# Performance work log

Measured on AMD Instinct MI355X. Metric: run time of the kernel, lower is better.

The kernel has to match this reference:

```python
import jax, jax.numpy as jnp
import numpy as np

ALPHA = 0.2          # LeakyReLU negative slope
NEG_INF = -9e15      # mask fill value, matches torch source
ADJ_EPS = 1e-6       # clamp min for log(adj)


def setup_inputs() -> dict:
    key = jax.random.key(0)
    k1, k2, k3, k4, k5 = jax.random.split(key, 5)
    N, F_IN, H, D = 4096, 256, 4, 64  # out_features = H*D = 256
    h = jax.random.normal(k1, (N, F_IN), dtype=jnp.float32)
    # xavier_uniform-ish scale for W (gain 1.414)
    limW = 1.414 * np.sqrt(6.0 / (F_IN + D))
    W = jax.random.uniform(k2, (H, F_IN, D), dtype=jnp.float32, minval=-limW, maxval=limW)
    lima = 1.414 * np.sqrt(6.0 / (D + 1))
    a_src = jax.random.uniform(k3, (H, D, 1), dtype=jnp.float32, minval=-lima, maxval=lima)
    a_dst = jax.random.uniform(k4, (H, D, 1), dtype=jnp.float32, minval=-lima, maxval=lima)
    # random 0/1 dense adjacency (float, as the torch module takes log(adj))
    adj = jax.random.randint(k5, (N, N), 0, 2).astype(jnp.float32)
    return {"h": h, "adj": adj, "W": W, "a_src": a_src, "a_dst": a_dst}


def reference(h, adj, W, a_src, a_dst):
    N = h.shape[0]
    # Wh: (H, N, D)
    Wh = jnp.einsum('ni,hid->hnd', h, W)
    # per-node source/dest scores: (H, N, 1)
    attn_src = jnp.einsum('hnd,hdo->hno', Wh, a_src)
    attn_dst = jnp.einsum('hnd,hdo->hno', Wh, a_dst)
    # broadcast to dense (H, N, N) logits
    e = jax.nn.leaky_relu(attn_src + jnp.swapaxes(attn_dst, -1, -2), negative_slope=ALPHA)
    adj_b = adj[None]  # (1, N, N)
    attention = jnp.where(adj_b > 0, e + jnp.log(jnp.maximum(adj_b, ADJ_EPS)), NEG_INF)
    attention = jax.nn.softmax(attention, axis=-1)
    # dropout p=0.0 (eval) -> identity
    h_prime = jnp.einsum('hnm,hmd->hnd', attention, Wh)        # (H, N, D)
    h_prime = jnp.transpose(h_prime, (1, 0, 2)).reshape(N, -1)  # (N, H*D)
    return jax.nn.elu(h_prime)  # concat=True branch
```

## Files before the change

kernel.cpp:

```cpp
#include <hip/hip_runtime.h>

typedef __attribute__((ext_vector_type(4))) float f32x4;
typedef __attribute__((ext_vector_type(8))) short short8;
typedef __attribute__((ext_vector_type(8))) __bf16 bf16x8;

constexpr int kN = 4096;
constexpr int kF = 256;
constexpr int kH = 4;
constexpr int kD = 64;
constexpr int kMP = 264;
constexpr float kLog2e = 1.4426950408889634f;

__device__ __forceinline__ unsigned short f2us(float x) {
  __bf16 b = (__bf16)x;
  return __builtin_bit_cast(unsigned short, b);
}

__global__ __launch_bounds__(256) void k_wh(const float* __restrict__ hmat,
                                            const float* __restrict__ W,
                                            const float* __restrict__ a_src,
                                            const float* __restrict__ a_dst,
                                            unsigned short* __restrict__ whb,
                                            float* __restrict__ s_src,
                                            float* __restrict__ s_dst,
                                            float* __restrict__ pmax) {
  const int h = blockIdx.x & 3, rb = blockIdx.x >> 2;
  const int row0 = rb * 64;
  const int t = threadIdx.x;
  __shared__ unsigned short wlds[16384];
  __shared__ float bm[4];
  {
    const int d = t & 63;
    const int dt = d >> 4, dl = d & 15;
    for (int kb = 0; kb < 64; kb++) {
      const int k = kb * 4 + (t >> 6);
      const float wv = W[((size_t)h * kF + k) * kD + d];
      const int ks = k >> 5, kl = k & 31;
      const int lane2 = ((kl >> 3) << 4) | dl;
      const int e = kl & 7;
      wlds[(((ks * 4 + dt) * 64 + lane2) << 3) + e] = f2us(wv);
    }
  }
  __syncthreads();
  const int wave = t >> 6, lane = t & 63;
  const int lr = lane & 15, lg = lane >> 4;
  const int nrow = row0 + wave * 16 + lr;
  f32x4 acc[4] = {};
  const float* hrow = hmat + (size_t)nrow * kF + 8 * lg;
#pragma unroll
  for (int ks = 0; ks < 8; ks++) {
    const f32x4 h0 = *reinterpret_cast<const f32x4*>(hrow + ks * 32);
    const f32x4 h1 = *reinterpret_cast<const f32x4*>(hrow + ks * 32 + 4);
    bf16x8 af;
#pragma unroll
    for (int j = 0; j < 4; j++) { af[j] = (__bf16)h0[j]; af[4 + j] = (__bf16)h1[j]; }
#pragma unroll
    for (int dt = 0; dt < 4; dt++) {
      const short8 bs = *reinterpret_cast<const short8*>(wlds + (((ks * 4 + dt) * 64 + lane) << 3));
      acc[dt] = __builtin_amdgcn_mfma_f32_16x16x32_bf16(af, __builtin_bit_cast(bf16x8, bs), acc[dt], 0, 0, 0);
    }
  }
#pragma unroll
  for (int dt = 0; dt < 4; dt++) {
#pragma unroll
    for (int r = 0; r < 4; r++) {
      const int n = row0 + wave * 16 + lg * 4 + r;
      const int mstep = n >> 5, kl = n & 31;
      const int lane2 = ((kl >> 3) << 4) | lr;
      const int e = kl & 7;
      whb[((((size_t)(h * 128 + mstep) * 4 + dt) * 64 + lane2) << 3) + e] = f2us(acc[dt][r]);
    }
  }
  float as4[4], ad4[4];
#pragma unroll
  for (int dt = 0; dt < 4; dt++) {
    as4[dt] = a_src[h * kD + dt * 16 + lr];
    ad4[dt] = a_dst[h * kD + dt * 16 + lr];
  }
  float wmax = -1e30f;
#pragma unroll
  for (int r = 0; r < 4; r++) {
    float ps = acc[0][r] * as4[0] + acc[1][r] * as4[1] + acc[2][r] * as4[2] + acc[3][r] * as4[3];
    float pd = acc[0][r] * ad4[0] + acc[1][r] * ad4[1] + acc[2][r] * ad4[2] + acc[3][r] * ad4[3];
#pragma unroll
    for (int off = 1; off < 16; off <<= 1) {
      ps += __shfl_xor(ps, off);
      pd += __shfl_xor(pd, off);
    }
    const int n = row0 + wave * 16 + lg * 4 + r;
    if (lr == 0) { s_src[h * kN + n] = ps; s_dst[h * kN + n] = pd; }
    wmax = fmaxf(wmax, pd);
  }
  wmax = fmaxf(wmax, __shfl_xor(wmax, 16));
  wmax = fmaxf(wmax, __shfl_xor(wmax, 32));
  if (lane == 0) bm[wave] = wmax;
  __syncthreads();
  if (t == 0)
    pmax[blockIdx.x] = fmaxf(fmaxf(bm[0], bm[1]), fmaxf(bm[2], bm[3]));
}

__device__ __forceinline__ float msel(float pv, unsigned m, int j) {
  const unsigned keep = (unsigned)(-(int)((m >> j) & 1u));
  return __builtin_bit_cast(float, __builtin_bit_cast(unsigned, pv) & keep);
}

__device__ __forceinline__ bf16x8 make_p2(const f32x4 E1a, const f32x4 E1b,
                                          const f32x4 E2a, const f32x4 E2b,
                                          const float K1, const float K2,
                                          const unsigned int m) {
  bf16x8 r;
#pragma unroll
  for (int j = 0; j < 4; j++)
    r[j] = (__bf16)msel(fmaxf(E1a[j] * K1, E2a[j] * K2), m, j);
#pragma unroll
  for (int j = 0; j < 4; j++)
    r[4 + j] = (__bf16)msel(fmaxf(E1b[j] * K1, E2b[j] * K2), m, 4 + j);
  return r;
}

__global__ __launch_bounds__(512, 4) void k_attn(const float* __restrict__ adj,
                                                 const unsigned short* __restrict__ whb,
                                                 const float* __restrict__ s_src,
                                                 const float* __restrict__ s_dst,
                                                 const float* __restrict__ pmax,
                                                 float* __restrict__ accP,
                                                 float* __restrict__ zP) {
  const int bid = blockIdx.x;
  const int rb = bid >> 2, cs = bid & 3;
  const int row0 = rb * 32;
  const int colbase = cs * 1024;
  const int t = threadIdx.x;
  const int wave = t >> 6, lane = t & 63;
  const int h = wave & 3, q = wave >> 2;
  const int lr = lane & 15, lg = lane >> 4;

  __shared__ float el1[4][1024];
  __shared__ float el2[4][1024];
  __shared__ unsigned char lmaskB[16 * kMP];
  __shared__ float zx[4][32];

  {
    f32x4 v[16];
    const float* abase = adj + (size_t)(row0 + wave * 4) * kN + colbase;
#pragma unroll
    for (int j = 0; j < 4; j++)
#pragma unroll
      for (int p = 0; p < 4; p++) {
        const int off = ((p >> 1) << 9) + 8 * lane + ((p & 1) << 2);
        v[j * 4 + p] = *reinterpret_cast<const f32x4*>(abase + (size_t)j * kN + off);
      }
#pragma unroll
    for (int j = 0; j < 4; j++) {
      const int rl = wave * 4 + j;
#pragma unroll
      for (int half = 0; half < 2; half++) {
        unsigned int b = 0;
#pragma unroll
        for (int i = 0; i < 4; i++) {
          b |= (v[j * 4 + half * 2][i] != 0.0f ? 1u : 0u) << i;
          b |= (v[j * 4 + half * 2 + 1][i] != 0.0f ? 1u : 0u) << (4 + i);
        }
        const int o = half * 64 + lane;
        lmaskB[(o >> 3) * kMP + rl * 8 + (o & 7)] = (unsigned char)b;
      }
    }
  }

#pragma unroll
  for (int j = 0; j < 2; j++) {
    const int idx = t + j * 512;
    const int hh = idx >> 8, c4 = (idx & 255) * 4;
    const f32x4 sd = *reinterpret_cast<const f32x4*>(s_dst + hh * kN + colbase + c4);
    f32x4 e1, e2;
#pragma unroll
    for (int i = 0; i < 4; i++) {
      const float u = sd[i] * kLog2e;
      e1[i] = __builtin_amdgcn_exp2f(u);
      e2[i] = __builtin_amdgcn_exp2f(0.2f * u);
    }
    *reinterpret_cast<f32x4*>(&el1[hh][c4]) = e1;
    *reinterpret_cast<f32x4*>(&el2[hh][c4]) = e2;
  }

  float M = pmax[(lane << 2) | h];
#pragma unroll
  for (int off = 1; off < 64; off <<= 1) M = fmaxf(M, __shfl_xor(M, off));

  float K1[2], K2[2];
#pragma unroll
  for (int rt = 0; rt < 2; rt++) {
    const float A = s_src[h * kN + row0 + rt * 16 + lr];
    const float xb = A + M;
    const float B = fmaxf(xb, 0.2f * xb);
    K1[rt] = __builtin_amdgcn_exp2f((A - B) * kLog2e);
    K2[rt] = __builtin_amdgcn_exp2f((0.2f * A - B) * kLog2e);
  }

  __syncthreads();

  const int Boff = (q << 2) | lg;
  unsigned int cw0[4], cw1[4];
#pragma unroll
  for (int w = 0; w < 4; w++) {
    unsigned int a0 = 0, a1 = 0;
#pragma unroll
    for (int d = 0; d < 4; d++) {
      const int c = w * 4 + d;
      a0 |= (unsigned int)lmaskB[c * kMP + lr * 8 + Boff] << (8 * d);
      a1 |= (unsigned int)lmaskB[c * kMP + (lr + 16) * 8 + Boff] << (8 * d);
    }
    cw0[w] = a0; cw1[w] = a1;
  }

  f32x4 acc0[4] = {}, acc1[4] = {};
  f32x4 accz0 = {}, accz1 = {};
  bf16x8 ones;
#pragma unroll
  for (int e = 0; e < 8; e++) ones[e] = (__bf16)1.0f;

  const float* e1p = &el1[h][q * 32 + 8 * lg];
  const float* e2p = &el2[h][q * 32 + 8 * lg];
  const short8* wb = reinterpret_cast<const short8*>(whb) + (size_t)h * 32768 + lane;
  const int mstep0 = cs * 32 + q;

  short8 bw[2][4];
#pragma unroll
  for (int sx = 0; sx < 2; sx++) {
    const short8* p = wb + (size_t)(mstep0 + sx * 2) * 256;
    bw[sx][0] = p[0]; bw[sx][1] = p[64]; bw[sx][2] = p[128]; bw[sx][3] = p[192];
  }

  f32x4 cE1a = *reinterpret_cast<const f32x4*>(e1p);
  f32x4 cE1b = *reinterpret_cast<const f32x4*>(e1p + 4);
  f32x4 cE2a = *reinterpret_cast<const f32x4*>(e2p);
  f32x4 cE2b = *reinterpret_cast<const f32x4*>(e2p + 4);

#pragma unroll
  for (int it = 0; it < 16; ++it) {
    const int nx = ((it + 1) & 15) * 64;
    const f32x4 nE1a = *reinterpret_cast<const f32x4*>(e1p + nx);
    const f32x4 nE1b = *reinterpret_cast<const f32x4*>(e1p + nx + 4);
    const f32x4 nE2a = *reinterpret_cast<const f32x4*>(e2p + nx);
    const f32x4 nE2b = *reinterpret_cast<const f32x4*>(e2p + nx + 4);

    const short8 cb0 = bw[it & 1][0], cb1 = bw[it & 1][1],
                 cb2 = bw[it & 1][2], cb3 = bw[it & 1][3];
    const short8* pp = wb + (size_t)(mstep0 + (it + 2) * 2) * 256;
    bw[it & 1][0] = pp[0];
    bw[it & 1][1] = pp[64];
    bw[it & 1][2] = pp[128];
    bw[it & 1][3] = pp[192];

    const unsigned cm0 = (cw0[it >> 2] >> ((it & 3) * 8)) & 0xFFu;
    const unsigned cm1 = (cw1[it >> 2] >> ((it & 3) * 8)) & 0xFFu;
    const bf16x8 P0 = make_p2(cE1a, cE1b, cE2a, cE2b, K1[0], K2[0], cm0);
    const bf16x8 P1 = make_p2(cE1a, cE1b, cE2a, cE2b, K1[1], K2[1], cm1);
    const bf16x8 B0 = __builtin_bit_cast(bf16x8, cb0);
    const bf16x8 B1 = __builtin_bit_cast(bf16x8, cb1);
    const bf16x8 B2 = __builtin_bit_cast(bf16x8, cb2);
    const bf16x8 B3 = __builtin_bit_cast(bf16x8, cb3);

    acc0[0] = __builtin_amdgcn_mfma_f32_16x16x32_bf16(P0, B0, acc0[0], 0, 0, 0);
    acc1[0] = __builtin_amdgcn_mfma_f32_16x16x32_bf16(P1, B0, acc1[0], 0, 0, 0);
    acc0[1] = __builtin_amdgcn_mfma_f32_16x16x32_bf16(P0, B1, acc0[1], 0, 0, 0);
    acc1[1] = __builtin_amdgcn_mfma_f32_16x16x32_bf16(P1, B1, acc1[1], 0, 0, 0);
    acc0[2] = __builtin_amdgcn_mfma_f32_16x16x32_bf16(P0, B2, acc0[2], 0, 0, 0);
    acc1[2] = __builtin_amdgcn_mfma_f32_16x16x32_bf16(P1, B2, acc1[2], 0, 0, 0);
    acc0[3] = __builtin_amdgcn_mfma_f32_16x16x32_bf16(P0, B3, acc0[3], 0, 0, 0);
    acc1[3] = __builtin_amdgcn_mfma_f32_16x16x32_bf16(P1, B3, acc1[3], 0, 0, 0);
    accz0 = __builtin_amdgcn_mfma_f32_16x16x32_bf16(P0, ones, accz0, 0, 0, 0);
    accz1 = __builtin_amdgcn_mfma_f32_16x16x32_bf16(P1, ones, accz1, 0, 0, 0);

    cE1a = nE1a; cE1b = nE1b; cE2a = nE2a; cE2b = nE2b;
  }

  __syncthreads();
  if (q == 1) {
#pragma unroll
    for (int dt = 0; dt < 4; dt++) {
      *reinterpret_cast<f32x4*>(&el1[h][(dt * 64 + lane) * 4]) = acc0[dt];
      *reinterpret_cast<f32x4*>(&el2[h][(dt * 64 + lane) * 4]) = acc1[dt];
    }
    if (lr == 0) {
#pragma unroll
      for (int r = 0; r < 4; r++) {
        zx[h][lg * 4 + r] = accz0[r];
        zx[h][16 + lg * 4 + r] = accz1[r];
      }
    }
  }
  __syncthreads();
  if (q == 0) {
#pragma unroll
    for (int dt = 0; dt < 4; dt++) {
      acc0[dt] += *reinterpret_cast<const f32x4*>(&el1[h][(dt * 64 + lane) * 4]);
      acc1[dt] += *reinterpret_cast<const f32x4*>(&el2[h][(dt * 64 + lane) * 4]);
    }
    const size_t ob = ((size_t)(cs * 4 + h) * kN + row0) * kD;
#pragma unroll
    for (int dt = 0; dt < 4; dt++)
#pragma unroll
      for (int r = 0; r < 4; r++) {
        accP[ob + (size_t)(lg * 4 + r) * kD + dt * 16 + lr] = acc0[dt][r];
        accP[ob + (size_t)(16 + lg * 4 + r) * kD + dt * 16 + lr] = acc1[dt][r];
      }
    if (lr == 0) {
      const size_t zb = (size_t)(cs * 4 + h) * kN + row0;
#pragma unroll
      for (int r = 0; r < 4; r++) {
        zP[zb + lg * 4 + r] = accz0[r] + zx[h][lg * 4 + r];
        zP[zb + 16 + lg * 4 + r] = accz1[r] + zx[h][16 + lg * 4 + r];
      }
    }
  }
}

__global__ __launch_bounds__(256) void k_fin(const float* __restrict__ accP,
                                             const float* __restrict__ zP,
                                             float* __restrict__ out) {
  const int idx = blockIdx.x * 256 + threadIdx.x;
  const int d4 = idx & 15;
  const int hh = (idx >> 4) & 3;
  const int n = idx >> 6;
  f32x4 v = {};
  float z = 0.0f;
#pragma unroll
  for (int s = 0; s < 4; s++) {
    v += reinterpret_cast<const f32x4*>(accP)[((size_t)(s * 4 + hh) * kN + n) * 16 + d4];
    z += zP[(size_t)(s * 4 + hh) * kN + n];
  }
  const float rz = 1.0f / z;
  f32x4 o;
#pragma unroll
  for (int j = 0; j < 4; j++) {
    const float x = v[j] * rz;
    o[j] = x > 0.0f ? x : (__builtin_amdgcn_exp2f(x * kLog2e) - 1.0f);
  }
  reinterpret_cast<f32x4*>(out)[(size_t)n * 64 + hh * 16 + d4] = o;
}

extern "C" void kernel_launch(void* const* d_in, const int* in_sizes, int n_in,
                              void* d_out, int out_size, void* d_ws, size_t ws_size,
                              hipStream_t stream) {
  const float* hmat  = (const float*)d_in[0];
  const float* adj   = (const float*)d_in[1];
  const float* W     = (const float*)d_in[2];
  const float* a_src = (const float*)d_in[3];
  const float* a_dst = (const float*)d_in[4];
  float* out = (float*)d_out;

  char* ws = (char*)d_ws;
  unsigned short* whb = (unsigned short*)(ws);
  float* s_src  = (float*)(ws + 0x200000);
  float* s_dst  = (float*)(ws + 0x210000);
  float* pmax   = (float*)(ws + 0x220000);
  float* accP   = (float*)(ws + 0x240000);
  float* zP     = (float*)(ws + 0x1240000);

  hipLaunchKernelGGL(k_wh, dim3(256), dim3(256), 0, stream,
                     hmat, W, a_src, a_dst, whb, s_src, s_dst, pmax);
  hipLaunchKernelGGL(k_attn, dim3(512), dim3(512), 0, stream,
                     adj, whb, s_src, s_dst, pmax, accP, zP);
  hipLaunchKernelGGL(k_fin, dim3(1024), dim3(256), 0, stream, accP, zP, out);
}
```

Measured before the change: 51.28 us.

## Split attention columns into eight chunks and halve shared memory per block

Doubles the column split of the attention kernel from 4 to 8 slices of 512 columns, launching 1024 blocks instead of 512. Per-block LDS for the exp tables and mask shrinks by half, and the cross-wave reduction is done in two passes so it fits the smaller buffers. The aim is more blocks, better occupancy and better load balance across CUs. In exchange the partial-sum buffer doubles, which adds global write and read traffic and makes the final kernel sum 8 partials.

Result: slower. 54.94 us (+7.2%).

```diff
diff --git a/kernel.cpp b/kernel.cpp
--- a/kernel.cpp
+++ b/kernel.cpp
@@ -126,50 +126,42 @@
                                                  float* __restrict__ accP,
                                                  float* __restrict__ zP) {
   const int bid = blockIdx.x;
-  const int rb = bid >> 2, cs = bid & 3;
+  const int rb = bid >> 3, cs = bid & 7;
   const int row0 = rb * 32;
-  const int colbase = cs * 1024;
+  const int colbase = cs * 512;
   const int t = threadIdx.x;
   const int wave = t >> 6, lane = t & 63;
   const int h = wave & 3, q = wave >> 2;
   const int lr = lane & 15, lg = lane >> 4;
 
-  __shared__ float el1[4][1024];
-  __shared__ float el2[4][1024];
-  __shared__ unsigned char lmaskB[16 * kMP];
+  __shared__ float el1[4][512];
+  __shared__ float el2[4][512];
+  __shared__ unsigned char lmaskB[8 * kMP];
   __shared__ float zx[4][32];
 
   {
-    f32x4 v[16];
-    const float* abase = adj + (size_t)(row0 + wave * 4) * kN + colbase;
+    f32x4 v[8];
+    const float* abase = adj + (size_t)(row0 + wave * 4) * kN + colbase + 8 * lane;
 #pragma unroll
     for (int j = 0; j < 4; j++)
 #pragma unroll
-      for (int p = 0; p < 4; p++) {
-        const int off = ((p >> 1) << 9) + 8 * lane + ((p & 1) << 2);
-        v[j * 4 + p] = *reinterpret_cast<const f32x4*>(abase + (size_t)j * kN + off);
-      }
+      for (int p = 0; p < 2; p++)
+        v[j * 2 + p] = *reinterpret_cast<const f32x4*>(abase + (size_t)j * kN + 4 * p);
 #pragma unroll
     for (int j = 0; j < 4; j++) {
       const int rl = wave * 4 + j;
-#pragma unroll
-      for (int half = 0; half < 2; half++) {
-        unsigned int b = 0;
-#pragma unroll
-        for (int i = 0; i < 4; i++) {
-          b |= (v[j * 4 + half * 2][i] != 0.0f ? 1u : 0u) << i;
-          b |= (v[j * 4 + half * 2 + 1][i] != 0.0f ? 1u : 0u) << (4 + i);
-        }
-        const int o = half * 64 + lane;
-        lmaskB[(o >> 3) * kMP + rl * 8 + (o & 7)] = (unsigned char)b;
+      unsigned int b = 0;
+#pragma unroll
+      for (int i = 0; i < 4; i++) {
+        b |= (v[j * 2][i] != 0.0f ? 1u : 0u) << i;
+        b |= (v[j * 2 + 1][i] != 0.0f ? 1u : 0u) << (4 + i);
       }
-    }
-  }
-
-#pragma unroll
-  for (int j = 0; j < 2; j++) {
-    const int idx = t + j * 512;
-    const int hh = idx >> 8, c4 = (idx & 255) * 4;
+      lmaskB[(lane >> 3) * kMP + rl * 8 + (lane & 7)] = (unsigned char)b;
+    }
+  }
+
+  {
+    const int hh = t >> 7, c4 = (t & 127) * 4;
     const f32x4 sd = *reinterpret_cast<const f32x4*>(s_dst + hh * kN + colbase + c4);
     f32x4 e1, e2;
 #pragma unroll
@@ -199,9 +191,9 @@
   __syncthreads();
 
   const int Boff = (q << 2) | lg;
-  unsigned int cw0[4], cw1[4];
-#pragma unroll
-  for (int w = 0; w < 4; w++) {
+  unsigned int cw0[2], cw1[2];
+#pragma unroll
+  for (int w = 0; w < 2; w++) {
     unsigned int a0 = 0, a1 = 0;
 #pragma unroll
     for (int d = 0; d < 4; d++) {
@@ -221,7 +213,7 @@
   const float* e1p = &el1[h][q * 32 + 8 * lg];
   const float* e2p = &el2[h][q * 32 + 8 * lg];
   const short8* wb = reinterpret_cast<const short8*>(whb) + (size_t)h * 32768 + lane;
-  const int mstep0 = cs * 32 + q;
+  const int mstep0 = cs * 16 + q;
 
   short8 bw[2][4];
 #pragma unroll
@@ -236,8 +228,8 @@
   f32x4 cE2b = *reinterpret_cast<const f32x4*>(e2p + 4);
 
 #pragma unroll
-  for (int it = 0; it < 16; ++it) {
-    const int nx = ((it + 1) & 15) * 64;
+  for (int it = 0; it < 8; ++it) {
+    const int nx = ((it + 1) & 7) * 64;
     const f32x4 nE1a = *reinterpret_cast<const f32x4*>(e1p + nx);
     const f32x4 nE1b = *reinterpret_cast<const f32x4*>(e1p + nx + 4);
     const f32x4 nE2a = *reinterpret_cast<const f32x4*>(e2p + nx);
@@ -274,12 +266,13 @@
     cE1a = nE1a; cE1b = nE1b; cE2a = nE2a; cE2b = nE2b;
   }
 
+  const size_t ob = ((size_t)(cs * 4 + h) * kN + row0) * kD;
   __syncthreads();
   if (q == 1) {
 #pragma unroll
-    for (int dt = 0; dt < 4; dt++) {
+    for (int dt = 0; dt < 2; dt++) {
       *reinterpret_cast<f32x4*>(&el1[h][(dt * 64 + lane) * 4]) = acc0[dt];
-      *reinterpret_cast<f32x4*>(&el2[h][(dt * 64 + lane) * 4]) = acc1[dt];
+      *reinterpret_cast<f32x4*>(&el2[h][(dt * 64 + lane) * 4]) = acc0[dt + 2];
     }
     if (lr == 0) {
 #pragma unroll
@@ -292,18 +285,36 @@
   __syncthreads();
   if (q == 0) {
 #pragma unroll
-    for (int dt = 0; dt < 4; dt++) {
+    for (int dt = 0; dt < 2; dt++) {
       acc0[dt] += *reinterpret_cast<const f32x4*>(&el1[h][(dt * 64 + lane) * 4]);
-      acc1[dt] += *reinterpret_cast<const f32x4*>(&el2[h][(dt * 64 + lane) * 4]);
-    }
-    const size_t ob = ((size_t)(cs * 4 + h) * kN + row0) * kD;
+      acc0[dt + 2] += *reinterpret_cast<const f32x4*>(&el2[h][(dt * 64 + lane) * 4]);
+    }
 #pragma unroll
     for (int dt = 0; dt < 4; dt++)
 #pragma unroll
-      for (int r = 0; r < 4; r++) {
+      for (int r = 0; r < 4; r++)
         accP[ob + (size_t)(lg * 4 + r) * kD + dt * 16 + lr] = acc0[dt][r];
+  }
+  __syncthreads();
+  if (q == 1) {
+#pragma unroll
+    for (int dt = 0; dt < 2; dt++) {
+      *reinterpret_cast<f32x4*>(&el1[h][(dt * 64 + lane) * 4]) = acc1[dt];
+      *reinterpret_cast<f32x4*>(&el2[h][(dt * 64 + lane) * 4]) = acc1[dt + 2];
+    }
+  }
+  __syncthreads();
+  if (q == 0) {
+#pragma unroll
+    for (int dt = 0; dt < 2; dt++) {
+      acc1[dt] += *reinterpret_cast<const f32x4*>(&el1[h][(dt * 64 + lane) * 4]);
+      acc1[dt + 2] += *reinterpret_cast<const f32x4*>(&el2[h][(dt * 64 + lane) * 4]);
+    }
+#pragma unroll
+    for (int dt = 0; dt < 4; dt++)
+#pragma unroll
+      for (int r = 0; r < 4; r++)
         accP[ob + (size_t)(16 + lg * 4 + r) * kD + dt * 16 + lr] = acc1[dt][r];
-      }
     if (lr == 0) {
       const size_t zb = (size_t)(cs * 4 + h) * kN + row0;
 #pragma unroll
@@ -325,7 +336,7 @@
   f32x4 v = {};
   float z = 0.0f;
 #pragma unroll
-  for (int s = 0; s < 4; s++) {
+  for (int s = 0; s < 8; s++) {
     v += reinterpret_cast<const f32x4*>(accP)[((size_t)(s * 4 + hh) * kN + n) * 16 + d4];
     z += zP[(size_t)(s * 4 + hh) * kN + n];
   }
@@ -355,11 +366,11 @@
   float* s_dst  = (float*)(ws + 0x210000);
   float* pmax   = (float*)(ws + 0x220000);
   float* accP   = (float*)(ws + 0x240000);
-  float* zP     = (float*)(ws + 0x1240000);
+  float* zP     = (float*)(ws + 0x2240000);
 
   hipLaunchKernelGGL(k_wh, dim3(256), dim3(256), 0, stream,
                      hmat, W, a_src, a_dst, whb, s_src, s_dst, pmax);
-  hipLaunchKernelGGL(k_attn, dim3(512), dim3(512), 0, stream,
+  hipLaunchKernelGGL(k_attn, dim3(1024), dim3(512), 0, stream,
                      adj, whb, s_src, s_dst, pmax, accP, zP);
   hipLaunchKernelGGL(k_fin, dim3(1024), dim3(256), 0, stream, accP, zP, out);
 }
```
